# Kernel tuning notes

Hardware: AMD Instinct MI355X
Metric: run time of the kernel (lower is better)

The kernel has to match this reference:

```python
import jax, jax.numpy as jnp
import numpy as np

H, T, D = 16, 2048, 1024
DH = D // H  # 64


def setup_inputs() -> dict:
    key = jax.random.key(0)
    ks = jax.random.split(key, 6)
    state = jax.random.normal(ks[0], (H, DH, DH), jnp.float32) * 0.02  # per-head recurrent state
    x = jax.random.normal(ks[1], (T, D), jnp.float32)
    done = jax.random.uniform(ks[2], (T,)) < (4.0 / T)  # sparse episode-reset flags (bool)
    w_qkv = jax.random.normal(ks[3], (D, 3 * D), jnp.float32) / np.sqrt(D)
    b_qkv = jnp.zeros((3 * D,), jnp.float32)
    w_out = jax.random.normal(ks[4], (D, D), jnp.float32) / np.sqrt(D)
    b_out = jnp.zeros((D,), jnp.float32)
    return {"state": state, "x": x, "done": done, "w_qkv": w_qkv,
            "b_qkv": b_qkv, "w_out": w_out, "b_out": b_out}


def _mha_forward(state, x, done, w_qkv, b_qkv, w_out, b_out):
    # qkv projection; einops 'T (QKV H Dh) -> QKV H T Dh'
    qkv = (x @ w_qkv + b_qkv).reshape(T, 3, H, DH).transpose(1, 2, 0, 3)
    q, k, v = qkv[0], qkv[1], qkv[2]  # each (H, T, Dh)

    cum = jnp.cumsum(done.astype(jnp.int32))  # inclusive cumsum, as in done.cumsum()
    before_first = cum == 0            # tokens before first reset (attend to carried state)
    after_last = cum == cum[-1]        # tokens after last reset (feed new state)
    done_any = cum[-1] > 0

    # make_attn_mask(done): causal AND no reset index i with s < i <= t.
    # The scanned mask equals: causal & (cum[t] == cum[s]) (same-segment).
    t_idx = jnp.arange(T)
    mask = (t_idx[:, None] >= t_idx[None, :]) & (cum[:, None] == cum[None, :])  # (T, T)

    attn = jnp.where(mask[None], jnp.einsum('htd,hsd->hts', q, k), 0.0)  # mask * (q @ k.T)
    q_bef = q * before_first[None, :, None]
    out = jnp.einsum('hts,hsd->htd', attn, v) + jnp.einsum('htd,hde->hte', q_bef, state)

    k_aft = k * after_last[None, :, None]
    v_aft = v * after_last[None, :, None]
    s_new = jnp.einsum('htd,hte->hde', k_aft, v_aft)  # k_aft.T @ v_aft per head
    new_state = jnp.where(done_any, s_new, state + s_new)

    # 'H T Dh -> T (H Dh)' then output projection
    x_out = out.transpose(1, 0, 2).reshape(T, D) @ w_out + b_out
    return new_state, x_out


def reference(state, x, done, w_qkv, b_qkv, w_out, b_out):
    return _mha_forward(state, x, done, w_qkv, b_qkv, w_out, b_out)
```

## Files before the change

kernel.cpp:

```cpp
#include <hip/hip_runtime.h>

#define TT 2048
#define DD 1024
#define HH 16
#define DH 64
#define QKV_N 3072
#define QKW 2048

typedef __attribute__((ext_vector_type(8))) short bf16x8;
typedef __attribute__((ext_vector_type(4))) short short4v;
typedef __attribute__((ext_vector_type(4))) float f32x4;

__device__ inline short f2bf(float f) {
    union { float f; unsigned u; } v; v.f = f;
    unsigned r = v.u + 0x7fff + ((v.u >> 16) & 1);
    return (short)(r >> 16);
}

__device__ inline f32x4 mfma16(bf16x8 a, bf16x8 b, f32x4 c) {
    return __builtin_amdgcn_mfma_f32_16x16x32_bf16(a, b, c, 0, 0, 0);
}

__device__ __forceinline__ void gload16(const void* g, void* l) {
    __builtin_amdgcn_global_load_lds(
        (const __attribute__((address_space(1))) unsigned int*)g,
        (__attribute__((address_space(3))) unsigned int*)l, 16, 0, 0);
}

__device__ void transpose_tile(const float* __restrict__ in, short* __restrict__ out,
                               int R, int C, int r0, int c0, float (*tile)[65]) {
    int tid = threadIdx.x;
#pragma unroll
    for (int p = 0; p < 4; ++p) {
        int ch = tid + p * 256;
        int r = ch >> 4, c4 = (ch & 15) * 4;
        float4 v = *(const float4*)&in[(size_t)(r0 + r) * C + c0 + c4];
        tile[r][c4] = v.x; tile[r][c4 + 1] = v.y; tile[r][c4 + 2] = v.z; tile[r][c4 + 3] = v.w;
    }
    __syncthreads();
#pragma unroll
    for (int p = 0; p < 2; ++p) {
        int ch = tid + p * 256;
        int c = ch >> 3, r8 = (ch & 7) * 8;
        short tmp[8];
#pragma unroll
        for (int i = 0; i < 8; ++i) tmp[i] = f2bf(tile[r8 + i][c]);
        *(float4*)&out[(size_t)(c0 + c) * R + r0 + r8] = *(float4*)tmp;
    }
}

__global__ __launch_bounds__(256) void prep_kernel(const float* __restrict__ x,
                                                   const float* __restrict__ w_qkv,
                                                   const float* __restrict__ w_out,
                                                   const float* __restrict__ state,
                                                   const int* __restrict__ done,
                                                   short* __restrict__ x_bf,
                                                   short* __restrict__ wqT,
                                                   short* __restrict__ woT,
                                                   short* __restrict__ stT,
                                                   float* __restrict__ stout,
                                                   int* __restrict__ seg,
                                                   int* __restrict__ totalp,
                                                   int* __restrict__ aux) {
    __shared__ float tile[64][65];
    __shared__ int scanbuf[2048 + 512 + 1];
    int b = blockIdx.x;
    int tid = threadIdx.x;
    if (b < 1024) {
        int i = (b * 256 + tid) * 8;
        float4 a = *(const float4*)&x[i];
        float4 c = *(const float4*)&x[i + 4];
        short tmp[8] = {f2bf(a.x), f2bf(a.y), f2bf(a.z), f2bf(a.w),
                        f2bf(c.x), f2bf(c.y), f2bf(c.z), f2bf(c.w)};
        *(float4*)&x_bf[i] = *(float4*)tmp;
    } else if (b < 1792) {
        int bb = b - 1024;
        transpose_tile(w_qkv, wqT, DD, QKV_N, (bb & 15) * 64, (bb >> 4) * 64, tile);
    } else if (b < 2048) {
        int bb = b - 1792;
        transpose_tile(w_out, woT, DD, DD, (bb & 15) * 64, (bb >> 4) * 64, tile);
    } else if (b < 2064) {
        int h = b - 2048;
        transpose_tile(state + (size_t)h * 4096, stT + (size_t)h * 4096, DH, DH, 0, 0, tile);
    } else if (b < 2128) {
        __shared__ int anyf;
        if (tid == 0) anyf = 0;
        __syncthreads();
        int acc = 0;
#pragma unroll
        for (int i = 0; i < 8; ++i) acc |= done[tid * 8 + i];
        if (acc) anyf = 1;
        __syncthreads();
        int f = ((b - 2064) * 256 + tid) * 4;
        float4 v = anyf ? make_float4(0.f, 0.f, 0.f, 0.f) : *(const float4*)&state[f];
        *(float4*)&stout[f] = v;
    } else {
        int* segl = scanbuf;
        int* part = scanbuf + 2048;
        int* excl = scanbuf + 2304;
        int base = tid * 8;
        int local[8];
        int run = 0;
#pragma unroll
        for (int i = 0; i < 8; ++i) { run += (done[base + i] != 0) ? 1 : 0; local[i] = run; }
        part[tid] = run;
        __syncthreads();
        if (tid < 64) {
            int p4[4];
#pragma unroll
            for (int i = 0; i < 4; ++i) p4[i] = part[tid * 4 + i];
            int s = p4[0] + p4[1] + p4[2] + p4[3];
            int v = s;
#pragma unroll
            for (int off = 1; off < 64; off <<= 1) {
                int u = __shfl_up(v, off);
                if (tid >= off) v += u;
            }
            int ex = v - s;
#pragma unroll
            for (int i = 0; i < 4; ++i) { excl[tid * 4 + i] = ex; ex += p4[i]; }
            if (tid == 63) { totalp[0] = v; scanbuf[2560] = v; }
        }
        __syncthreads();
        int off = excl[tid];
#pragma unroll
        for (int i = 0; i < 8; ++i) {
            int sv = off + local[i];
            seg[base + i] = sv;
            segl[base + i] = sv;
        }
        __syncthreads();
        if (tid < 33) {
            int target = (tid < 32) ? segl[tid * 64] : scanbuf[2560];
            int lo = 0, hi = 2047;
            while (lo < hi) { int mid = (lo + hi) >> 1; if (segl[mid] >= target) hi = mid; else lo = mid + 1; }
            aux[tid] = lo >> 6;
        }
    }
}

__global__ __launch_bounds__(256) void gemm_qkv(const short* __restrict__ A,
                                                const short* __restrict__ BT,
                                                const float* __restrict__ bias,
                                                short* __restrict__ qk,
                                                short* __restrict__ vt) {
    __shared__ short As[128 * 32];
    __shared__ short Bs[128 * 32];
    const int K = DD;
    int tid = threadIdx.x;
    int wave = tid >> 6, lane = tid & 63;
    int quad = lane >> 4, l15 = lane & 15;
    int m0 = blockIdx.x * 128, n0 = blockIdx.y * 128;
    int wr = (wave >> 1) * 64, wc = (wave & 1) * 64;

    int srow = wave * 16 + (lane >> 2);
    int scol = (lane & 3) * 8;
    const short* Ag = A + (size_t)(m0 + srow) * K + scol;
    const short* Bg = BT + (size_t)(n0 + srow) * K + scol;
    short* As0 = &As[(wave * 16) * 32];
    short* As1 = &As[(64 + wave * 16) * 32];
    short* Bs0 = &Bs[(wave * 16) * 32];
    short* Bs1 = &Bs[(64 + wave * 16) * 32];

    f32x4 acc[4][4] = {};
    for (int k0 = 0; k0 < K; k0 += 32) {
        __syncthreads();
        gload16(Ag + k0, As0);
        gload16(Ag + (size_t)64 * K + k0, As1);
        gload16(Bg + k0, Bs0);
        gload16(Bg + (size_t)64 * K + k0, Bs1);
        __syncthreads();
        bf16x8 af[4], bfr[4];
#pragma unroll
        for (int i = 0; i < 4; ++i) {
            af[i]  = *(const bf16x8*)&As[(wr + i * 16 + l15) * 32 + quad * 8];
            bfr[i] = *(const bf16x8*)&Bs[(wc + i * 16 + l15) * 32 + quad * 8];
        }
#pragma unroll
        for (int i = 0; i < 4; ++i)
#pragma unroll
            for (int j = 0; j < 4; ++j)
                acc[i][j] = mfma16(af[i], bfr[j], acc[i][j]);
    }

    if (n0 < 2048) {
#pragma unroll
        for (int i = 0; i < 4; ++i)
#pragma unroll
            for (int j = 0; j < 4; ++j)
#pragma unroll
                for (int r = 0; r < 4; ++r) {
                    int row = m0 + wr + i * 16 + quad * 4 + r;
                    int col = n0 + wc + j * 16 + l15;
                    qk[(size_t)row * QKW + col] = f2bf(acc[i][j][r] + bias[col]);
                }
    } else {
#pragma unroll
        for (int j = 0; j < 4; ++j) {
            int col = n0 + wc + j * 16 + l15;
            float bv = bias[col];
            int eg = col - 2048;
            int hh = eg >> 6, e = eg & 63;
#pragma unroll
            for (int i = 0; i < 4; ++i) {
                int tb = m0 + wr + i * 16 + quad * 4;
                short4v pk;
#pragma unroll
                for (int r = 0; r < 4; ++r) pk[r] = f2bf(acc[i][j][r] + bv);
                *(short4v*)&vt[(size_t)hh * (DH * TT) + (size_t)e * TT + tb] = pk;
            }
        }
    }
}

__global__ __launch_bounds__(256) void attn_mfma(const short* __restrict__ qk,
                                                 const short* __restrict__ vt,
                                                 const short* __restrict__ stT,
                                                 const int* __restrict__ seg,
                                                 const int* __restrict__ totalp,
                                                 const int* __restrict__ aux,
                                                 short* __restrict__ outb,
                                                 float* __restrict__ part,
                                                 float* __restrict__ nsout) {
    __shared__ short Ss_lo[64 * 32];
    __shared__ short Ss_hi[64 * 32];

    int h = blockIdx.x, tt = blockIdx.y, sc = blockIdx.z;
    int t0 = tt * 64;
    int tid = threadIdx.x, wave = tid >> 6, lane = tid & 63;
    int quad = lane >> 4, l15 = lane & 15;
    int myt = wave * 16;
    const short* vbase = vt + (size_t)h * (DH * TT);

    if (sc == 4) {
        if (tt < aux[32]) return;
        int total = totalp[0];
        int myd = myt;
        {
            bool keep = (seg[t0 + lane] == total);
            const short* src = qk + (size_t)(t0 + lane) * QKW + 1024 + h * DH + myd;
            union { float4 f; short s[8]; } u0, u1;
            u0.f = keep ? *(const float4*)src : make_float4(0.f, 0.f, 0.f, 0.f);
            u1.f = keep ? *(const float4*)(src + 8) : make_float4(0.f, 0.f, 0.f, 0.f);
            short* dst = (lane < 32) ? &Ss_lo[lane] : &Ss_hi[lane - 32];
#pragma unroll
            for (int i = 0; i < 8; ++i) {
                dst[(myd + i) * 32] = u0.s[i];
                dst[(myd + 8 + i) * 32] = u1.s[i];
            }
        }
        bf16x8 a0 = *(const bf16x8*)&Ss_lo[(myd + l15) * 32 + quad * 8];
        bf16x8 a1 = *(const bf16x8*)&Ss_hi[(myd + l15) * 32 + quad * 8];
        f32x4 acc[4] = {};
#pragma unroll
        for (int j = 0; j < 4; ++j) {
            const short* vrow = vbase + (size_t)(j * 16 + l15) * TT + t0 + quad * 8;
            bf16x8 b0 = *(const bf16x8*)vrow;
            bf16x8 b1 = *(const bf16x8*)(vrow + 32);
            acc[j] = mfma16(a0, b0, acc[j]);
            acc[j] = mfma16(a1, b1, acc[j]);
        }
        float* oh = nsout + (size_t)h * 4096;
#pragma unroll
        for (int j = 0; j < 4; ++j)
#pragma unroll
            for (int r = 0; r < 4; ++r)
                atomicAdd(&oh[(myd + quad * 4 + r) * DH + j * 16 + l15], acc[j][r]);
        return;
    }

    int st0 = aux[tt];
    int sc_lo = st0 >> 3, sc_hi = tt >> 3;
    if (sc < sc_lo || sc > sc_hi) return;
    bool direct = (sc_lo == sc_hi);
    int st_lo = (st0 > sc * 8) ? st0 : sc * 8;
    int st_hi = (tt < sc * 8 + 7) ? tt : sc * 8 + 7;

    const short* qrow = qk + (size_t)(t0 + myt + l15) * QKW + h * DH + quad * 8;
    bf16x8 qf0 = *(const bf16x8*)qrow;
    bf16x8 qf1 = *(const bf16x8*)(qrow + 32);

    int tlane = t0 + myt + l15;
    int seg_lane = seg[tlane];
    int segt_r[4];
#pragma unroll
    for (int r = 0; r < 4; ++r) segt_r[r] = seg[t0 + myt + quad * 4 + r];

    f32x4 accT[4] = {};
    if (sc == sc_lo && seg[t0] == 0) {
        const short* sb = stT + (size_t)h * 4096;
#pragma unroll
        for (int j = 0; j < 4; ++j) {
            const short* srow = sb + (j * 16 + l15) * 64 + quad * 8;
            bf16x8 a0 = *(const bf16x8*)srow;
            bf16x8 a1 = *(const bf16x8*)(srow + 32);
            accT[j] = mfma16(a0, qf0, accT[j]);
            accT[j] = mfma16(a1, qf1, accT[j]);
        }
        if (seg_lane != 0) {
#pragma unroll
            for (int j = 0; j < 4; ++j)
#pragma unroll
                for (int r = 0; r < 4; ++r) accT[j][r] = 0.f;
        }
    }

    short* ss_lo = &Ss_lo[myt * 32];
    short* ss_hi = &Ss_hi[myt * 32];
    const short* kbase = qk + 1024 + h * DH;

    for (int st = st_lo; st <= st_hi; ++st) {
        int s0 = st * 64;
        int segv[4];
#pragma unroll
        for (int j = 0; j < 4; ++j) segv[j] = seg[s0 + j * 16 + l15];
        bf16x8 kb0[4], kb1[4];
#pragma unroll
        for (int j = 0; j < 4; ++j) {
            const short* krow = kbase + (size_t)(s0 + j * 16 + l15) * QKW + quad * 8;
            kb0[j] = *(const bf16x8*)krow;
            kb1[j] = *(const bf16x8*)(krow + 32);
        }
        bf16x8 va0[4], va1[4];
#pragma unroll
        for (int j = 0; j < 4; ++j) {
            const short* vrow = vbase + (size_t)(j * 16 + l15) * TT + s0 + quad * 8;
            va0[j] = *(const bf16x8*)vrow;
            va1[j] = *(const bf16x8*)(vrow + 32);
        }
        f32x4 sacc[4] = {};
#pragma unroll
        for (int j = 0; j < 4; ++j) {
            sacc[j] = mfma16(qf0, kb0[j], sacc[j]);
            sacc[j] = mfma16(qf1, kb1[j], sacc[j]);
        }
        bool last = (st == tt);
#pragma unroll
        for (int j = 0; j < 4; ++j) {
            int sgl = s0 + j * 16 + l15;
#pragma unroll
            for (int r = 0; r < 4; ++r) {
                bool ok = (segv[j] == segt_r[r]);
                if (last) ok = ok && (sgl <= t0 + myt + quad * 4 + r);
                short v = ok ? f2bf(sacc[j][r]) : (short)0;
                int row = quad * 4 + r;
                if (j < 2) ss_lo[row * 32 + j * 16 + l15] = v;
                else       ss_hi[row * 32 + (j - 2) * 16 + l15] = v;
            }
        }
        bf16x8 sf0 = *(const bf16x8*)&ss_lo[l15 * 32 + quad * 8];
        bf16x8 sf1 = *(const bf16x8*)&ss_hi[l15 * 32 + quad * 8];
#pragma unroll
        for (int j = 0; j < 4; ++j) {
            accT[j] = mfma16(va0[j], sf0, accT[j]);
            accT[j] = mfma16(va1[j], sf1, accT[j]);
        }
    }

    if (direct) {
#pragma unroll
        for (int j = 0; j < 4; ++j) {
            short4v pk;
#pragma unroll
            for (int r = 0; r < 4; ++r) pk[r] = f2bf(accT[j][r]);
            *(short4v*)&outb[(size_t)tlane * DD + h * DH + j * 16 + quad * 4] = pk;
        }
    } else {
        float* pb = part + (((size_t)(h * 32 + tt) * 4 + sc) * 4096);
#pragma unroll
        for (int j = 0; j < 4; ++j)
            *(f32x4*)&pb[(myt + l15) * 64 + j * 16 + quad * 4] = accT[j];
    }
}

__global__ __launch_bounds__(256) void attn_reduce(const float* __restrict__ part,
                                                   const int* __restrict__ aux,
                                                   short* __restrict__ outb) {
    int h = blockIdx.x, tt = blockIdx.y;
    int sc_lo = aux[tt] >> 3, sc_hi = tt >> 3;
    if (sc_lo == sc_hi) return;
    int t0 = tt * 64;
    int tid = threadIdx.x;
    int tl16 = tid >> 4, e4 = (tid & 15) * 4;
    const float* pb = part + ((size_t)(h * 32 + tt) * 4) * 4096;
#pragma unroll
    for (int p = 0; p < 4; ++p) {
        int tl = p * 16 + tl16;
        float4 acc = make_float4(0.f, 0.f, 0.f, 0.f);
        for (int sc = sc_lo; sc <= sc_hi; ++sc) {
            float4 v = *(const float4*)&pb[sc * 4096 + tl * 64 + e4];
            acc.x += v.x; acc.y += v.y; acc.z += v.z; acc.w += v.w;
        }
        short4v pk;
        pk[0] = f2bf(acc.x); pk[1] = f2bf(acc.y); pk[2] = f2bf(acc.z); pk[3] = f2bf(acc.w);
        *(short4v*)&outb[(size_t)(t0 + tl) * DD + h * DH + e4] = pk;
    }
}

__global__ __launch_bounds__(256) void gemm_out(const short* __restrict__ A,
                                                const short* __restrict__ BT,
                                                const float* __restrict__ bias,
                                                float* __restrict__ Cout,
                                                int M, int N, int K) {
    __shared__ short As[128 * 32];
    __shared__ short Bs[128 * 32];
    int tid = threadIdx.x;
    int wave = tid >> 6, lane = tid & 63;
    int quad = lane >> 4, l15 = lane & 15;
    int m0 = blockIdx.x * 128, n0 = blockIdx.y * 128;
    int wr = (wave >> 1) * 64, wc = (wave & 1) * 64;

    int srow = wave * 16 + (lane >> 2);
    int scol = (lane & 3) * 8;
    const short* Ag = A + (size_t)(m0 + srow) * K + scol;
    const short* Bg = BT + (size_t)(n0 + srow) * K + scol;
    short* As0 = &As[(wave * 16) * 32];
    short* As1 = &As[(64 + wave * 16) * 32];
    short* Bs0 = &Bs[(wave * 16) * 32];
    short* Bs1 = &Bs[(64 + wave * 16) * 32];

    f32x4 acc[4][4] = {};
    for (int k0 = 0; k0 < K; k0 += 32) {
        __syncthreads();
        gload16(Ag + k0, As0);
        gload16(Ag + (size_t)64 * K + k0, As1);
        gload16(Bg + k0, Bs0);
        gload16(Bg + (size_t)64 * K + k0, Bs1);
        __syncthreads();
        bf16x8 af[4], bfr[4];
#pragma unroll
        for (int i = 0; i < 4; ++i) {
            af[i]  = *(const bf16x8*)&As[(wr + i * 16 + l15) * 32 + quad * 8];
            bfr[i] = *(const bf16x8*)&Bs[(wc + i * 16 + l15) * 32 + quad * 8];
        }
#pragma unroll
        for (int i = 0; i < 4; ++i)
#pragma unroll
            for (int j = 0; j < 4; ++j)
                acc[i][j] = mfma16(af[i], bfr[j], acc[i][j]);
    }
#pragma unroll
    for (int i = 0; i < 4; ++i)
#pragma unroll
        for (int j = 0; j < 4; ++j)
#pragma unroll
            for (int r = 0; r < 4; ++r) {
                int row = m0 + wr + i * 16 + quad * 4 + r;
                int col = n0 + wc + j * 16 + l15;
                Cout[(size_t)row * N + col] = acc[i][j][r] + bias[col];
            }
}

extern "C" void kernel_launch(void* const* d_in, const int* in_sizes, int n_in,
                              void* d_out, int out_size, void* d_ws, size_t ws_size,
                              hipStream_t stream) {
    const float* state = (const float*)d_in[0];
    const float* x     = (const float*)d_in[1];
    const int*   done  = (const int*)d_in[2];
    const float* w_qkv = (const float*)d_in[3];
    const float* b_qkv = (const float*)d_in[4];
    const float* w_out = (const float*)d_in[5];
    const float* b_out = (const float*)d_in[6];

    char* ws = (char*)d_ws;
    int*   seg    = (int*)ws;
    int*   totalp = (int*)(ws + 8192);
    int*   aux    = (int*)(ws + 8256);
    short* wqT    = (short*)(ws + 8448);
    short* woT    = (short*)(ws + 6299904);
    short* stT    = (short*)(ws + 8397056);
    short* qk     = (short*)(ws + 8528128);
    short* vt     = (short*)(ws + 16916736);
    short* xbf_outb = (short*)(ws + 21111040);
    float* part   = (float*)(ws + 25305344);

    float* new_state_out = (float*)d_out;
    float* x_out         = (float*)d_out + HH * DH * DH;

    prep_kernel<<<2129, 256, 0, stream>>>(x, w_qkv, w_out, state, done,
                                          xbf_outb, wqT, woT, stT,
                                          new_state_out, seg, totalp, aux);

    gemm_qkv<<<dim3(TT / 128, QKV_N / 128), 256, 0, stream>>>(
        xbf_outb, wqT, b_qkv, qk, vt);

    attn_mfma<<<dim3(HH, TT / 64, 5), 256, 0, stream>>>(
        qk, vt, stT, seg, totalp, aux, xbf_outb, part, new_state_out);

    attn_reduce<<<dim3(HH, TT / 64), 256, 0, stream>>>(part, aux, xbf_outb);

    gemm_out<<<dim3(TT / 128, DD / 128), 256, 0, stream>>>(
        xbf_outb, woT, b_out, x_out, TT, DD, DD);
}
```

Baseline: 180.3 us.

## Enlarge attention query tile to 128 rows and stage K/V in LDS

The attention kernel now processes 128 query rows per block instead of 64, with each wave handling 32 rows. Q, K and V tiles are staged into shared memory with direct global-to-LDS loads, so the four waves share each K/V tile instead of each loading it separately. The reduce kernel and partial-buffer indexing are resized to match. This halves the grid and increases per-block LDS use and barriers, which may lower occupancy, and output stores become scalar rather than vectorised.

```diff
diff --git a/kernel.cpp b/kernel.cpp
--- a/kernel.cpp
+++ b/kernel.cpp
@@ -144,8 +144,8 @@
                                                 const float* __restrict__ bias,
                                                 short* __restrict__ qk,
                                                 short* __restrict__ vt) {
-    __shared__ short As[128 * 32];
-    __shared__ short Bs[128 * 32];
+    __shared__ __align__(16) short As[128 * 32];
+    __shared__ __align__(16) short Bs[128 * 32];
     const int K = DD;
     int tid = threadIdx.x;
     int wave = tid >> 6, lane = tid & 63;
@@ -222,178 +222,211 @@
                                                  short* __restrict__ outb,
                                                  float* __restrict__ part,
                                                  float* __restrict__ nsout) {
-    __shared__ short Ss_lo[64 * 32];
-    __shared__ short Ss_hi[64 * 32];
-
-    int h = blockIdx.x, tt = blockIdx.y, sc = blockIdx.z;
-    int t0 = tt * 64;
+    __shared__ __align__(16) short Kh[2][64 * 32];
+    __shared__ __align__(16) short Vh[2][64 * 32];
+    __shared__ __align__(16) short Qh[2][128 * 32];
+    __shared__ __align__(16) short Ss[128 * 72];
+
+    int h = blockIdx.x, tb = blockIdx.y, sc = blockIdx.z;
+    int t0 = tb * 128;
     int tid = threadIdx.x, wave = tid >> 6, lane = tid & 63;
     int quad = lane >> 4, l15 = lane & 15;
-    int myt = wave * 16;
+    int myt = wave * 32;
     const short* vbase = vt + (size_t)h * (DH * TT);
 
     if (sc == 4) {
-        if (tt < aux[32]) return;
         int total = totalp[0];
-        int myd = myt;
-        {
-            bool keep = (seg[t0 + lane] == total);
-            const short* src = qk + (size_t)(t0 + lane) * QKW + 1024 + h * DH + myd;
+        int myd = wave * 16;
+#pragma unroll
+        for (int cc = 0; cc < 2; ++cc) {
+            int ct = tb * 2 + cc;
+            if (ct < aux[32]) continue;
+            int t0c = ct * 64;
+            bool keep = (seg[t0c + lane] == total);
+            const short* src = qk + (size_t)(t0c + lane) * QKW + 1024 + h * DH + myd;
             union { float4 f; short s[8]; } u0, u1;
             u0.f = keep ? *(const float4*)src : make_float4(0.f, 0.f, 0.f, 0.f);
             u1.f = keep ? *(const float4*)(src + 8) : make_float4(0.f, 0.f, 0.f, 0.f);
-            short* dst = (lane < 32) ? &Ss_lo[lane] : &Ss_hi[lane - 32];
+            short* dst = (lane < 32) ? &Kh[0][lane] : &Kh[1][lane - 32];
 #pragma unroll
             for (int i = 0; i < 8; ++i) {
                 dst[(myd + i) * 32] = u0.s[i];
                 dst[(myd + 8 + i) * 32] = u1.s[i];
             }
-        }
-        bf16x8 a0 = *(const bf16x8*)&Ss_lo[(myd + l15) * 32 + quad * 8];
-        bf16x8 a1 = *(const bf16x8*)&Ss_hi[(myd + l15) * 32 + quad * 8];
-        f32x4 acc[4] = {};
-#pragma unroll
-        for (int j = 0; j < 4; ++j) {
-            const short* vrow = vbase + (size_t)(j * 16 + l15) * TT + t0 + quad * 8;
-            bf16x8 b0 = *(const bf16x8*)vrow;
-            bf16x8 b1 = *(const bf16x8*)(vrow + 32);
-            acc[j] = mfma16(a0, b0, acc[j]);
-            acc[j] = mfma16(a1, b1, acc[j]);
-        }
-        float* oh = nsout + (size_t)h * 4096;
-#pragma unroll
-        for (int j = 0; j < 4; ++j)
-#pragma unroll
-            for (int r = 0; r < 4; ++r)
-                atomicAdd(&oh[(myd + quad * 4 + r) * DH + j * 16 + l15], acc[j][r]);
+            bf16x8 a0 = *(const bf16x8*)&Kh[0][(myd + l15) * 32 + quad * 8];
+            bf16x8 a1 = *(const bf16x8*)&Kh[1][(myd + l15) * 32 + quad * 8];
+            f32x4 acc2[4] = {};
+#pragma unroll
+            for (int j = 0; j < 4; ++j) {
+                const short* vrow = vbase + (size_t)(j * 16 + l15) * TT + t0c + quad * 8;
+                bf16x8 b0 = *(const bf16x8*)vrow;
+                bf16x8 b1 = *(const bf16x8*)(vrow + 32);
+                acc2[j] = mfma16(a0, b0, acc2[j]);
+                acc2[j] = mfma16(a1, b1, acc2[j]);
+            }
+            float* oh = nsout + (size_t)h * 4096;
+#pragma unroll
+            for (int j = 0; j < 4; ++j)
+#pragma unroll
+                for (int r = 0; r < 4; ++r)
+                    atomicAdd(&oh[(myd + quad * 4 + r) * DH + j * 16 + l15], acc2[j][r]);
+        }
         return;
     }
 
-    int st0 = aux[tt];
-    int sc_lo = st0 >> 3, sc_hi = tt >> 3;
+    int st0 = aux[2 * tb];
+    int sc_lo = st0 >> 3, sc_hi = (2 * tb + 1) >> 3;
     if (sc < sc_lo || sc > sc_hi) return;
     bool direct = (sc_lo == sc_hi);
     int st_lo = (st0 > sc * 8) ? st0 : sc * 8;
-    int st_hi = (tt < sc * 8 + 7) ? tt : sc * 8 + 7;
-
-    const short* qrow = qk + (size_t)(t0 + myt + l15) * QKW + h * DH + quad * 8;
-    bf16x8 qf0 = *(const bf16x8*)qrow;
-    bf16x8 qf1 = *(const bf16x8*)(qrow + 32);
-
-    int tlane = t0 + myt + l15;
-    int seg_lane = seg[tlane];
-    int segt_r[4];
-#pragma unroll
-    for (int r = 0; r < 4; ++r) segt_r[r] = seg[t0 + myt + quad * 4 + r];
-
-    f32x4 accT[4] = {};
+    int st_hi = (2 * tb + 1 < sc * 8 + 7) ? 2 * tb + 1 : sc * 8 + 7;
+
+    {
+        int srow = (lane >> 2);
+        int chunk = (lane & 3);
+#pragma unroll
+        for (int h2 = 0; h2 < 2; ++h2)
+#pragma unroll
+            for (int q = 0; q < 2; ++q) {
+                int row = myt + q * 16 + srow;
+                gload16(qk + (size_t)(t0 + row) * QKW + h * DH + h2 * 32 + chunk * 8,
+                        &Qh[h2][(myt + q * 16) * 32]);
+            }
+    }
+    __syncthreads();
+
+    bf16x8 af[2][2];
+#pragma unroll
+    for (int i = 0; i < 2; ++i)
+#pragma unroll
+        for (int h2 = 0; h2 < 2; ++h2)
+            af[i][h2] = *(const bf16x8*)&Qh[h2][(myt + i * 16 + l15) * 32 + quad * 8];
+
+    int tg[2][4], segt[2][4];
+#pragma unroll
+    for (int i = 0; i < 2; ++i)
+#pragma unroll
+        for (int r = 0; r < 4; ++r) {
+            tg[i][r] = t0 + myt + i * 16 + quad * 4 + r;
+            segt[i][r] = seg[tg[i][r]];
+        }
+
+    f32x4 acc[2][4] = {};
     if (sc == sc_lo && seg[t0] == 0) {
         const short* sb = stT + (size_t)h * 4096;
 #pragma unroll
-        for (int j = 0; j < 4; ++j) {
-            const short* srow = sb + (j * 16 + l15) * 64 + quad * 8;
-            bf16x8 a0 = *(const bf16x8*)srow;
-            bf16x8 a1 = *(const bf16x8*)(srow + 32);
-            accT[j] = mfma16(a0, qf0, accT[j]);
-            accT[j] = mfma16(a1, qf1, accT[j]);
-        }
-        if (seg_lane != 0) {
-#pragma unroll
-            for (int j = 0; j < 4; ++j)
-#pragma unroll
-                for (int r = 0; r < 4; ++r) accT[j][r] = 0.f;
-        }
-    }
-
-    short* ss_lo = &Ss_lo[myt * 32];
-    short* ss_hi = &Ss_hi[myt * 32];
-    const short* kbase = qk + 1024 + h * DH;
+        for (int j = 0; j < 4; ++j)
+#pragma unroll
+            for (int h2 = 0; h2 < 2; ++h2) {
+                bf16x8 b = *(const bf16x8*)(sb + (j * 16 + l15) * 64 + h2 * 32 + quad * 8);
+#pragma unroll
+                for (int i = 0; i < 2; ++i)
+                    acc[i][j] = mfma16(af[i][h2], b, acc[i][j]);
+            }
+#pragma unroll
+        for (int i = 0; i < 2; ++i)
+#pragma unroll
+            for (int r = 0; r < 4; ++r)
+                if (segt[i][r] != 0)
+#pragma unroll
+                    for (int j = 0; j < 4; ++j) acc[i][j][r] = 0.f;
+    }
+
+    int srow = wave * 16 + (lane >> 2);
+    int chunk = (lane & 3);
+    const short* kg = qk + 1024 + h * DH;
 
     for (int st = st_lo; st <= st_hi; ++st) {
         int s0 = st * 64;
-        int segv[4];
-#pragma unroll
-        for (int j = 0; j < 4; ++j) segv[j] = seg[s0 + j * 16 + l15];
-        bf16x8 kb0[4], kb1[4];
-#pragma unroll
-        for (int j = 0; j < 4; ++j) {
-            const short* krow = kbase + (size_t)(s0 + j * 16 + l15) * QKW + quad * 8;
-            kb0[j] = *(const bf16x8*)krow;
-            kb1[j] = *(const bf16x8*)(krow + 32);
-        }
-        bf16x8 va0[4], va1[4];
-#pragma unroll
-        for (int j = 0; j < 4; ++j) {
-            const short* vrow = vbase + (size_t)(j * 16 + l15) * TT + s0 + quad * 8;
-            va0[j] = *(const bf16x8*)vrow;
-            va1[j] = *(const bf16x8*)(vrow + 32);
-        }
-        f32x4 sacc[4] = {};
-#pragma unroll
-        for (int j = 0; j < 4; ++j) {
-            sacc[j] = mfma16(qf0, kb0[j], sacc[j]);
-            sacc[j] = mfma16(qf1, kb1[j], sacc[j]);
-        }
-        bool last = (st == tt);
-#pragma unroll
-        for (int j = 0; j < 4; ++j) {
-            int sgl = s0 + j * 16 + l15;
-#pragma unroll
-            for (int r = 0; r < 4; ++r) {
-                bool ok = (segv[j] == segt_r[r]);
-                if (last) ok = ok && (sgl <= t0 + myt + quad * 4 + r);
-                short v = ok ? f2bf(sacc[j][r]) : (short)0;
-                int row = quad * 4 + r;
-                if (j < 2) ss_lo[row * 32 + j * 16 + l15] = v;
-                else       ss_hi[row * 32 + (j - 2) * 16 + l15] = v;
-            }
-        }
-        bf16x8 sf0 = *(const bf16x8*)&ss_lo[l15 * 32 + quad * 8];
-        bf16x8 sf1 = *(const bf16x8*)&ss_hi[l15 * 32 + quad * 8];
-#pragma unroll
-        for (int j = 0; j < 4; ++j) {
-            accT[j] = mfma16(va0[j], sf0, accT[j]);
-            accT[j] = mfma16(va1[j], sf1, accT[j]);
-        }
+        __syncthreads();
+        gload16(kg + (size_t)(s0 + srow) * QKW + chunk * 8,        &Kh[0][(wave * 16) * 32]);
+        gload16(kg + (size_t)(s0 + srow) * QKW + 32 + chunk * 8,   &Kh[1][(wave * 16) * 32]);
+        gload16(vbase + (size_t)srow * TT + s0 + chunk * 8,        &Vh[0][(wave * 16) * 32]);
+        gload16(vbase + (size_t)srow * TT + s0 + 32 + chunk * 8,   &Vh[1][(wave * 16) * 32]);
+        __syncthreads();
+
+        int segs[4], sg[4];
+#pragma unroll
+        for (int j = 0; j < 4; ++j) { sg[j] = s0 + j * 16 + l15; segs[j] = seg[sg[j]]; }
+
+        f32x4 sacc[2][4] = {};
+#pragma unroll
+        for (int j = 0; j < 4; ++j)
+#pragma unroll
+            for (int h2 = 0; h2 < 2; ++h2) {
+                bf16x8 kb = *(const bf16x8*)&Kh[h2][(j * 16 + l15) * 32 + quad * 8];
+#pragma unroll
+                for (int i = 0; i < 2; ++i)
+                    sacc[i][j] = mfma16(af[i][h2], kb, sacc[i][j]);
+            }
+#pragma unroll
+        for (int i = 0; i < 2; ++i)
+#pragma unroll
+            for (int j = 0; j < 4; ++j)
+#pragma unroll
+                for (int r = 0; r < 4; ++r) {
+                    bool ok = (segs[j] == segt[i][r]) && (sg[j] <= tg[i][r]);
+                    Ss[(myt + i * 16 + quad * 4 + r) * 72 + j * 16 + l15] =
+                        ok ? f2bf(sacc[i][j][r]) : (short)0;
+                }
+        bf16x8 sf[2][2];
+#pragma unroll
+        for (int i = 0; i < 2; ++i)
+#pragma unroll
+            for (int h2 = 0; h2 < 2; ++h2)
+                sf[i][h2] = *(const bf16x8*)&Ss[(myt + i * 16 + l15) * 72 + h2 * 32 + quad * 8];
+#pragma unroll
+        for (int j = 0; j < 4; ++j)
+#pragma unroll
+            for (int h2 = 0; h2 < 2; ++h2) {
+                bf16x8 vb = *(const bf16x8*)&Vh[h2][(j * 16 + l15) * 32 + quad * 8];
+#pragma unroll
+                for (int i = 0; i < 2; ++i)
+                    acc[i][j] = mfma16(sf[i][h2], vb, acc[i][j]);
+            }
     }
 
     if (direct) {
 #pragma unroll
-        for (int j = 0; j < 4; ++j) {
-            short4v pk;
-#pragma unroll
-            for (int r = 0; r < 4; ++r) pk[r] = f2bf(accT[j][r]);
-            *(short4v*)&outb[(size_t)tlane * DD + h * DH + j * 16 + quad * 4] = pk;
-        }
+        for (int i = 0; i < 2; ++i)
+#pragma unroll
+            for (int j = 0; j < 4; ++j)
+#pragma unroll
+                for (int r = 0; r < 4; ++r)
+                    outb[(size_t)tg[i][r] * DD + h * DH + j * 16 + l15] = f2bf(acc[i][j][r]);
     } else {
-        float* pb = part + (((size_t)(h * 32 + tt) * 4 + sc) * 4096);
-#pragma unroll
-        for (int j = 0; j < 4; ++j)
-            *(f32x4*)&pb[(myt + l15) * 64 + j * 16 + quad * 4] = accT[j];
+        float* pb = part + ((size_t)((h * 16 + tb) * 4 + sc)) * 8192;
+#pragma unroll
+        for (int i = 0; i < 2; ++i)
+#pragma unroll
+            for (int j = 0; j < 4; ++j)
+#pragma unroll
+                for (int r = 0; r < 4; ++r)
+                    pb[(myt + i * 16 + quad * 4 + r) * 64 + j * 16 + l15] = acc[i][j][r];
     }
 }
 
 __global__ __launch_bounds__(256) void attn_reduce(const float* __restrict__ part,
                                                    const int* __restrict__ aux,
                                                    short* __restrict__ outb) {
-    int h = blockIdx.x, tt = blockIdx.y;
-    int sc_lo = aux[tt] >> 3, sc_hi = tt >> 3;
+    int h = blockIdx.x, tb = blockIdx.y;
+    int sc_lo = aux[2 * tb] >> 3, sc_hi = (2 * tb + 1) >> 3;
     if (sc_lo == sc_hi) return;
-    int t0 = tt * 64;
+    int t0 = tb * 128;
     int tid = threadIdx.x;
-    int tl16 = tid >> 4, e4 = (tid & 15) * 4;
-    const float* pb = part + ((size_t)(h * 32 + tt) * 4) * 4096;
-#pragma unroll
-    for (int p = 0; p < 4; ++p) {
-        int tl = p * 16 + tl16;
+    const float* pb = part + ((size_t)(h * 16 + tb) * 4) * 8192;
+#pragma unroll
+    for (int p = 0; p < 8; ++p) {
+        int idx = p * 256 + tid;
+        int row = idx >> 4, c4 = (idx & 15) * 4;
         float4 acc = make_float4(0.f, 0.f, 0.f, 0.f);
         for (int sc = sc_lo; sc <= sc_hi; ++sc) {
-            float4 v = *(const float4*)&pb[sc * 4096 + tl * 64 + e4];
+            float4 v = *(const float4*)&pb[(size_t)sc * 8192 + row * 64 + c4];
             acc.x += v.x; acc.y += v.y; acc.z += v.z; acc.w += v.w;
         }
         short4v pk;
         pk[0] = f2bf(acc.x); pk[1] = f2bf(acc.y); pk[2] = f2bf(acc.z); pk[3] = f2bf(acc.w);
-        *(short4v*)&outb[(size_t)(t0 + tl) * DD + h * DH + e4] = pk;
+        *(short4v*)&outb[(size_t)(t0 + row) * DD + h * DH + c4] = pk;
     }
 }
 
@@ -402,8 +435,8 @@
                                                 const float* __restrict__ bias,
                                                 float* __restrict__ Cout,
                                                 int M, int N, int K) {
-    __shared__ short As[128 * 32];
-    __shared__ short Bs[128 * 32];
+    __shared__ __align__(16) short As[128 * 32];
+    __shared__ __align__(16) short Bs[128 * 32];
     int tid = threadIdx.x;
     int wave = tid >> 6, lane = tid & 63;
     int quad = lane >> 4, l15 = lane & 15;
@@ -484,10 +517,10 @@
     gemm_qkv<<<dim3(TT / 128, QKV_N / 128), 256, 0, stream>>>(
         xbf_outb, wqT, b_qkv, qk, vt);
 
-    attn_mfma<<<dim3(HH, TT / 64, 5), 256, 0, stream>>>(
+    attn_mfma<<<dim3(HH, TT / 128, 5), 256, 0, stream>>>(
         qk, vt, stT, seg, totalp, aux, xbf_outb, part, new_state_out);
 
-    attn_reduce<<<dim3(HH, TT / 64), 256, 0, stream>>>(part, aux, xbf_outb);
+    attn_reduce<<<dim3(HH, TT / 128), 256, 0, stream>>>(part, aux, xbf_outb);
 
     gemm_out<<<dim3(TT / 128, DD / 128), 256, 0, stream>>>(
         xbf_outb, woT, b_out, x_out, TT, DD, DD);
```

Measured after the change: 161.9 us. 1.11x faster.
